# Kernel tuning notes

Hardware: AMD Instinct MI355X
Metric: run time of the kernel (lower is better)

## Reference

```python
import jax, jax.numpy as jnp
import numpy as np

N, E, D, L, G = 50000, 600000, 128, 3, 512
MAX_DIS = 5
BN_EPS = 1e-5


def _bn(z, g, b):
    # BatchNorm1d in training mode: biased batch statistics over axis 0
    mu = jnp.mean(z, axis=0)
    var = jnp.var(z, axis=0)
    return (z - mu) * jax.lax.rsqrt(var + BN_EPS) * g + b


def setup_inputs() -> dict:
    key = jax.random.key(0)
    ks = jax.random.split(key, 16)
    s = 0.05
    inp = {
        # int inputs
        'd': jax.random.randint(ks[0], (N,), 0, MAX_DIS + 1, dtype=jnp.int32),
        'src': jax.random.randint(ks[1], (E,), 0, N, dtype=jnp.int32),
        'dst': jax.random.randint(ks[2], (E,), 0, N, dtype=jnp.int32),
        'batch_ids': jnp.sort(jax.random.randint(ks[3], (N,), 0, G, dtype=jnp.int32)),
        # NodeEmbedding distance table
        'embed_d': jax.random.normal(ks[4], (MAX_DIS + 1, D)) * s,
        # per-layer params (stacked over L layers)
        'lin_W': jax.random.normal(ks[5], (L, D, D)) * s,   # self.linear weight (stored [in,out])
        'lin_b': jnp.zeros((L, D)),                          # self.linear bias
        'mlp_W1': jax.random.normal(ks[6], (L, D, D)) * s,   # MLP input linear (no bias, norm=True)
        'mlp_g1': jnp.ones((L, D)), 'mlp_b1': jnp.zeros((L, D)),  # MLP inner BN
        'mlp_W2': jax.random.normal(ks[7], (L, D, D)) * s,   # MLP output linear (no bias)
        'eps': jnp.zeros((L,)),                              # GIN eps per layer
        'bn_g': jnp.ones((L, D)), 'bn_b': jnp.zeros((L, D)), # LWL outer BN
        # Pool (gin=False, task='g')
        'pool_W1': jax.random.normal(ks[8], (D, D)) * s,
        'pool_g1': jnp.ones((D,)), 'pool_b1': jnp.zeros((D,)),
        'pool_W2': jax.random.normal(ks[9], (D, D)) * s,
        'pbn_g': jnp.ones((D,)), 'pbn_b': jnp.zeros((D,)),
        # predict MLP (norm=False -> biases, hdim=2*D, odim=num_tasks*num_classes=1)
        'pred_W1': jax.random.normal(ks[10], (D, 2 * D)) * s,
        'pred_b1': jnp.zeros((2 * D,)),
        'pred_W2': jax.random.normal(ks[11], (2 * D, 1)) * s,
        'pred_b2': jnp.zeros((1,)),
    }
    return inp


def reference(d, src, dst, batch_ids, embed_d, lin_W, lin_b,
              mlp_W1, mlp_g1, mlp_b1, mlp_W2, eps, bn_g, bn_b,
              pool_W1, pool_g1, pool_b1, pool_W2, pbn_g, pbn_b,
              pred_W1, pred_b1, pred_W2, pred_b2):
    # NodeEmbedding: x = embed_d(clamp(d, 0, max_dis))  (enc_a=None -> no feature encoder)
    x = embed_d[jnp.clip(d, 0, MAX_DIS)]                      # [N, D]

    counts = jax.ops.segment_sum(jnp.ones((N,), x.dtype), batch_ids, num_segments=G)
    denom = jnp.maximum(counts, 1.0)[:, None]                 # [G, 1]

    h_means = []
    for l in range(L):
        # L('vL'): message = relu(index_select(linear(x), src))  (enc_e=None)
        m = jax.nn.relu((x @ lin_W[l] + lin_b[l])[src])        # [E, D]
        # aggregate = scatter_add to dst over N nodes
        agg = jax.ops.segment_sum(m, dst, num_segments=N)      # [N, D]
        z = x * (1.0 + eps[l]) + agg                           # GIN eps residual
        # MLP(norm=True): Linear(no bias) -> BN -> ReLU -> Linear(no bias)
        h = jax.nn.relu(_bn(z @ mlp_W1[l], mlp_g1[l], mlp_b1[l])) @ mlp_W2[l]
        # LWL outer: x = relu(bn(xL))
        x = jax.nn.relu(_bn(h, bn_g[l], bn_b[l]))
        # global_mean_pool of this layer's output
        h_means.append(jax.ops.segment_sum(x, batch_ids, num_segments=G) / denom)

    # Pool (gin=False, task='g'); index_u is identity for plain MP, so scatter/gather are no-ops
    p = jax.nn.relu(_bn(x @ pool_W1, pool_g1, pool_b1)) @ pool_W2   # pooling MLP
    p = jax.nn.relu(_bn(p, pbn_g, pbn_b))
    h_graph = jax.ops.segment_sum(p, batch_ids, num_segments=G) / denom  # scatter mean
    # predict MLP (norm=False): Linear+bias -> ReLU -> Linear+bias
    prediction = jax.nn.relu(h_graph @ pred_W1 + pred_b1) @ pred_W2 + pred_b2  # [G, 1]

    return prediction, h_graph, jnp.stack(h_means)  # h_list stacked [L, G, D]
```

## Files before the change

kernel.cpp:

```cpp
#include <hip/hip_runtime.h>

typedef unsigned short ushort_t;
typedef __attribute__((ext_vector_type(8))) short bf16x8;
typedef __attribute__((ext_vector_type(4))) float f32x4;

#define NN 50000
#define NE 600000
#define DD 128
#define LL 3
#define GG 512
#define NB_SCAN 98
#define GGRID 782
#define SBK 16

__device__ __forceinline__ float b2f(ushort_t u){ return __uint_as_float(((unsigned)u)<<16); }
__device__ __forceinline__ ushort_t f2b(float f){
    unsigned x = __float_as_uint(f);
    return (ushort_t)((x + 0x7fffu + ((x>>16)&1u)) >> 16);
}

__global__ void k_mark(float* __restrict__ out, float val, int n){
    int i = blockIdx.x*256 + threadIdx.x; if (i >= n) return;
    out[i] = (i == 0) ? val : 0.f;
}

struct WPtrs { const float* p[11]; };
__global__ void k_setup(WPtrs wp, ushort_t* __restrict__ Wf,
                        const int* __restrict__ bids, int* __restrict__ goff,
                        int* __restrict__ cnt, float* __restrict__ banks,
                        const float* __restrict__ emb, const float* __restrict__ linW,
                        const float* __restrict__ linB, float* __restrict__ yrows){
    int idx = blockIdx.x*256 + threadIdx.x;
    if (idx < 180224){
        int m = idx >> 14, r = idx & 16383;
        int i = r & 7, l2 = (r >> 3) & 63, s = (r >> 9) & 3, n = r >> 11;
        int k   = s*32 + (l2 >> 4)*8 + i;
        int col = n*16 + (l2 & 15);
        Wf[idx] = f2b(wp.p[m][k*DD + col]);
    } else if (idx < 180737){
        int g = idx - 180224;
        int lo = 0, hi = NN;
        while (lo < hi){ int mid = (lo+hi) >> 1; if (bids[mid] < g) lo = mid+1; else hi = mid; }
        goff[g] = lo;
    } else if (idx < 230737){
        cnt[idx - 180737] = 0;
    } else if (idx < 263505){
        banks[idx - 230737] = 0.f;
    } else if (idx < 264273){
        int i = idx - 263505;
        int di = i >> 7, c = i & 127;
        float acc = linB[c];
        for (int k = 0; k < DD; k++) acc = fmaf(emb[di*DD + k], linW[k*DD + c], acc);
        yrows[i] = fmaxf(acc, 0.f);
    }
}

__global__ void k_count(const int* __restrict__ dst, int* __restrict__ cnt){
    int e4 = blockIdx.x*256 + threadIdx.x; if (e4 >= NE/4) return;
    int4 dv = ((const int4*)dst)[e4];
    atomicAdd(&cnt[dv.x], 1); atomicAdd(&cnt[dv.y], 1);
    atomicAdd(&cnt[dv.z], 1); atomicAdd(&cnt[dv.w], 1);
}
__global__ void k_scanA(const int* __restrict__ cnt, int* __restrict__ inc, int* __restrict__ bsum){
    __shared__ int s[512];
    int i = blockIdx.x*512 + threadIdx.x;
    int v = (i < NN) ? cnt[i] : 0;
    s[threadIdx.x] = v; __syncthreads();
    for (int off = 1; off < 512; off <<= 1){
        int add = (threadIdx.x >= off) ? s[threadIdx.x - off] : 0;
        __syncthreads();
        s[threadIdx.x] += add;
        __syncthreads();
    }
    if (i < NN) inc[i] = s[threadIdx.x];
    if (threadIdx.x == 511) bsum[blockIdx.x] = s[511];
}
__global__ void k_scanB(const int* __restrict__ bsum, int* __restrict__ boff){
    __shared__ int s[128];
    int t = threadIdx.x;
    int v = (t < NB_SCAN) ? bsum[t] : 0;
    s[t] = v; __syncthreads();
    for (int off = 1; off < 128; off <<= 1){
        int a = (t >= off) ? s[t - off] : 0;
        __syncthreads();
        s[t] += a;
        __syncthreads();
    }
    if (t < NB_SCAN) boff[t] = s[t] - v;
    if (t == NB_SCAN - 1) boff[NB_SCAN] = s[t];
}
__global__ void k_scanC(const int* __restrict__ cnt, const int* __restrict__ inc,
                        const int* __restrict__ boff, int* __restrict__ rowptr,
                        int* __restrict__ cursor){
    int i = blockIdx.x*512 + threadIdx.x;
    if (i < NN){
        int e = boff[blockIdx.x] + inc[i] - cnt[i];
        rowptr[i] = e; cursor[i] = e;
    } else if (i == NN){
        rowptr[NN] = NE;
    }
}
__global__ void k_fill(const int* __restrict__ src, const int* __restrict__ dst,
                       int* __restrict__ cursor, int* __restrict__ eidx){
    int e4 = blockIdx.x*256 + threadIdx.x; if (e4 >= NE/4) return;
    int4 dv = ((const int4*)dst)[e4];
    int4 sv = ((const int4*)src)[e4];
    int p0 = atomicAdd(&cursor[dv.x], 1); eidx[p0] = sv.x;
    int p1 = atomicAdd(&cursor[dv.y], 1); eidx[p1] = sv.y;
    int p2 = atomicAdd(&cursor[dv.z], 1); eidx[p2] = sv.z;
    int p3 = atomicAdd(&cursor[dv.w], 1); eidx[p3] = sv.w;
}

__global__ void k_agg0(const int* __restrict__ d, const float* __restrict__ emb,
                       const float* __restrict__ yrows,
                       const int* __restrict__ rowptr, const int* __restrict__ eidx,
                       const float* __restrict__ epsP, ushort_t* __restrict__ zb){
    __shared__ float eL[6*DD], yL[6*DD];
    int t = threadIdx.x;
    for (int i = t; i < 6*DD; i += 256){ eL[i] = emb[i]; yL[i] = yrows[i]; }
    __syncthreads();
    int node = blockIdx.x*16 + (t >> 4);
    if (node >= NN) return;
    int c8 = (t & 15) << 3;
    float epl = 1.0f + epsP[0];
    int dv = d[node]; dv = dv < 0 ? 0 : (dv > 5 ? 5 : dv);
    float a[8];
#pragma unroll
    for (int i = 0; i < 8; i++) a[i] = eL[dv*DD + c8 + i] * epl;
    int e0 = rowptr[node], e1 = rowptr[node+1];
    int e = e0;
    for (; e + 3 < e1; e += 4){
        int s0 = eidx[e], s1 = eidx[e+1], s2 = eidx[e+2], s3 = eidx[e+3];
        int c0 = d[s0], c1 = d[s1], c2 = d[s2], c3 = d[s3];
        c0 = c0 < 0 ? 0 : (c0 > 5 ? 5 : c0);
        c1 = c1 < 0 ? 0 : (c1 > 5 ? 5 : c1);
        c2 = c2 < 0 ? 0 : (c2 > 5 ? 5 : c2);
        c3 = c3 < 0 ? 0 : (c3 > 5 ? 5 : c3);
#pragma unroll
        for (int i = 0; i < 8; i++)
            a[i] += (yL[c0*DD + c8 + i] + yL[c1*DD + c8 + i])
                  + (yL[c2*DD + c8 + i] + yL[c3*DD + c8 + i]);
    }
    for (; e < e1; e++){
        int s = eidx[e];
        int c = d[s]; c = c < 0 ? 0 : (c > 5 ? 5 : c);
#pragma unroll
        for (int i = 0; i < 8; i++) a[i] += yL[c*DD + c8 + i];
    }
    bf16x8 o;
#pragma unroll
    for (int i = 0; i < 8; i++) o[i] = (short)f2b(a[i]);
    *(bf16x8*)(zb + (size_t)node*DD + c8) = o;
}

__global__ void k_agg(const ushort_t* __restrict__ xb, const ushort_t* __restrict__ yb,
                      ushort_t* __restrict__ zb,
                      const int* __restrict__ rowptr, const int* __restrict__ eidx,
                      const float* __restrict__ epsP, int l,
                      const float* __restrict__ banksIn, const float* __restrict__ bng,
                      const float* __restrict__ bnb){
    __shared__ float sst[256];
    int t = threadIdx.x;
    {
        float sv = 0.f;
#pragma unroll
        for (int b = 0; b < SBK; b++) sv += banksIn[(b << 8) + t];
        sst[t] = sv;
    }
    __syncthreads();
    int node = blockIdx.x*16 + (t >> 4);
    if (node >= NN) return;
    int c8 = (t & 15) << 3;
    float epl = 1.0f + epsP[l];
    bf16x8 xr = *(const bf16x8*)(xb + (size_t)node*DD + c8);
    float a[8];
#pragma unroll
    for (int i = 0; i < 8; i++){
        int c = c8 + i;
        float mu  = sst[c] * (1.0f/NN);
        float var = sst[c + DD] * (1.0f/NN) - mu*mu;
        float sc  = rsqrtf(fmaxf(var, 0.f) + 1e-5f) * bng[c];
        float sh  = bnb[c] - mu*sc;
        a[i] = fmaxf(fmaf(b2f((ushort_t)xr[i]), sc, sh), 0.f) * epl;
    }
    int e0 = rowptr[node], e1 = rowptr[node+1];
    int e = e0;
    for (; e + 3 < e1; e += 4){
        int s0 = eidx[e], s1 = eidx[e+1], s2 = eidx[e+2], s3 = eidx[e+3];
        bf16x8 v0 = *(const bf16x8*)(yb + (size_t)s0*DD + c8);
        bf16x8 v1 = *(const bf16x8*)(yb + (size_t)s1*DD + c8);
        bf16x8 v2 = *(const bf16x8*)(yb + (size_t)s2*DD + c8);
        bf16x8 v3 = *(const bf16x8*)(yb + (size_t)s3*DD + c8);
#pragma unroll
        for (int i = 0; i < 8; i++)
            a[i] += (b2f((ushort_t)v0[i]) + b2f((ushort_t)v1[i]))
                  + (b2f((ushort_t)v2[i]) + b2f((ushort_t)v3[i]));
    }
    for (; e < e1; e++){
        int s = eidx[e];
        bf16x8 v = *(const bf16x8*)(yb + (size_t)s*DD + c8);
#pragma unroll
        for (int i = 0; i < 8; i++) a[i] += b2f((ushort_t)v[i]);
    }
    bf16x8 o;
#pragma unroll
    for (int i = 0; i < 8; i++) o[i] = (short)f2b(a[i]);
    *(bf16x8*)(zb + (size_t)node*DD + c8) = o;
}

template<int AMODE, int OMODE, int STATS, int POOL>
__global__ __launch_bounds__(256) void k_gemm(
    const ushort_t* __restrict__ A, const ushort_t* __restrict__ Wf,
    const float* __restrict__ bias,
    const float* __restrict__ banksIn, const float* __restrict__ bng,
    const float* __restrict__ bnb,
    ushort_t* __restrict__ C, float* __restrict__ banksOut,
    const int* __restrict__ goff, float* __restrict__ pool_out, int M)
{
    __shared__ float ssl[256];
    __shared__ float sred[256];
    __shared__ float lrep[64*132];
    const int t = threadIdx.x;

    if (POOL && blockIdx.x >= GGRID){
        int g = blockIdx.x - GGRID;
        {
            float sv = 0.f;
#pragma unroll
            for (int b = 0; b < SBK; b++) sv += banksIn[(b << 8) + t];
            ssl[t] = sv;
        }
        __syncthreads();
        int c = t & 127, hf = t >> 7;
        float mu  = ssl[c] * (1.0f/NN);
        float var = ssl[c + DD] * (1.0f/NN) - mu*mu;
        float sc  = rsqrtf(fmaxf(var, 0.f) + 1e-5f) * bng[c];
        float sh  = bnb[c] - mu*sc;
        int r0 = goff[g], r1 = goff[g+1];
        float acc = 0.f;
        for (int r = r0 + hf; r < r1; r += 2)
            acc += fmaxf(fmaf(b2f(A[(size_t)r*DD + c]), sc, sh), 0.f);
        sred[t] = acc; __syncthreads();
        if (t < 128)
            pool_out[g*DD + t] = (sred[t] + sred[t+128]) / fmaxf((float)(r1 - r0), 1.0f);
        return;
    }

    const int w = t >> 6, l = t & 63;
    const int rowBlk = blockIdx.x*64, rowBase = rowBlk + w*16;
    const int lm = l & 15, kg = l >> 4;

    if (AMODE == 2){
        float sv = 0.f;
#pragma unroll
        for (int b = 0; b < SBK; b++) sv += banksIn[(b << 8) + t];
        ssl[t] = sv;
        __syncthreads();
        if (t < 128){
            float mu  = ssl[t] * (1.0f/NN);
            float var = ssl[t + DD] * (1.0f/NN) - mu*mu;
            float sc  = rsqrtf(fmaxf(var, 0.f) + 1e-5f) * bng[t];
            ssl[t] = sc;
            ssl[t + DD] = bnb[t] - mu*sc;
        }
    }
    if (STATS) sred[t] = 0.f;
    if (AMODE == 2 || STATS) __syncthreads();

    f32x4 acc[8];
#pragma unroll
    for (int n = 0; n < 8; n++) acc[n] = (f32x4){0.f,0.f,0.f,0.f};

    int arow = rowBase + lm;
    if (arow >= M) arow = M - 1;
    const ushort_t* aptr = A + (size_t)arow*DD + kg*8;

#pragma unroll
    for (int s = 0; s < 4; s++){
        bf16x8 af;
        if (AMODE == 0){
            af = *(const bf16x8*)(aptr + s*32);
        } else {
            bf16x8 ar = *(const bf16x8*)(aptr + s*32);
            int k0 = s*32 + kg*8;
#pragma unroll
            for (int i = 0; i < 8; i++){
                float v = b2f((ushort_t)ar[i]);
                v = fmaxf(fmaf(v, ssl[k0+i], ssl[DD+k0+i]), 0.f);
                ((ushort_t*)&af)[i] = f2b(v);
            }
        }
#pragma unroll
        for (int n = 0; n < 8; n++){
            bf16x8 bfr = *(const bf16x8*)(Wf + (size_t)((n*4 + s)*64 + l)*8);
            acc[n] = __builtin_amdgcn_mfma_f32_16x16x32_bf16(af, bfr, acc[n], 0, 0, 0);
        }
    }

#pragma unroll
    for (int n = 0; n < 8; n++){
        int col = n*16 + lm;
        float cs = 0.f, cq = 0.f;
#pragma unroll
        for (int j = 0; j < 4; j++){
            float v = acc[n][j];
            if (OMODE == 1) v = fmaxf(v + bias[col], 0.f);
            lrep[(w*16 + kg*4 + j)*132 + col] = v;
            if (STATS && (rowBase + kg*4 + j) < M){ cs += v; cq += v*v; }
        }
        if (STATS){
            cs += __shfl_xor(cs, 16); cs += __shfl_xor(cs, 32);
            cq += __shfl_xor(cq, 16); cq += __shfl_xor(cq, 32);
            if (kg == 0){
                atomicAdd(&sred[col], cs);
                atomicAdd(&sred[col + DD], cq);
            }
        }
    }
    __syncthreads();

    {
        int lr = t & 63;
        int gr = rowBlk + lr;
        if (gr < M){
            int seg = (t >> 6) * 32;
            const float* lp = lrep + lr*132 + seg;
            bf16x8 o0, o1, o2, o3;
#pragma unroll
            for (int i = 0; i < 8; i++){
                o0[i] = (short)f2b(lp[i]);
                o1[i] = (short)f2b(lp[8+i]);
                o2[i] = (short)f2b(lp[16+i]);
                o3[i] = (short)f2b(lp[24+i]);
            }
            ushort_t* cp = C + (size_t)gr*DD + seg;
            *(bf16x8*)(cp)      = o0;
            *(bf16x8*)(cp + 8)  = o1;
            *(bf16x8*)(cp + 16) = o2;
            *(bf16x8*)(cp + 24) = o3;
        }
    }

    if (STATS){
        __syncthreads();
        atomicAdd(&banksOut[((blockIdx.x & (SBK-1)) << 8) + t], sred[t]);
    }
}

__global__ __launch_bounds__(256) void k_poolpred(const ushort_t* __restrict__ zb,
        const float* __restrict__ banksIn, const float* __restrict__ bng,
        const float* __restrict__ bnb, const int* __restrict__ goff,
        const float* __restrict__ W1, const float* __restrict__ b1,
        const float* __restrict__ W2, const float* __restrict__ b2,
        float* __restrict__ out_hgraph, float* __restrict__ out_pred){
    __shared__ float hrow[DD];
    __shared__ float pr[256];
    int g = blockIdx.x, t = threadIdx.x;
    {
        float sv = 0.f;
#pragma unroll
        for (int b = 0; b < SBK; b++) sv += banksIn[(b << 8) + t];
        pr[t] = sv;
    }
    __syncthreads();
    int c = t & 127, hf = t >> 7;
    float mu  = pr[c] * (1.0f/NN);
    float var = pr[c + DD] * (1.0f/NN) - mu*mu;
    float sc  = rsqrtf(fmaxf(var, 0.f) + 1e-5f) * bng[c];
    float sh  = bnb[c] - mu*sc;
    __syncthreads();
    int r0 = goff[g], r1 = goff[g+1];
    float acc = 0.f;
    for (int r = r0 + hf; r < r1; r += 2)
        acc += fmaxf(fmaf(b2f(zb[(size_t)r*DD + c]), sc, sh), 0.f);
    pr[t] = acc; __syncthreads();
    if (t < 128){
        float m = (pr[t] + pr[t+128]) / fmaxf((float)(r1 - r0), 1.0f);
        hrow[t] = m;
        out_hgraph[g*DD + t] = m;
    }
    __syncthreads();
    float a2 = b1[t];
    for (int k = 0; k < DD; k++) a2 = fmaf(hrow[k], W1[k*256 + t], a2);
    pr[t] = fmaxf(a2, 0.f) * W2[t];
    __syncthreads();
    for (int off = 128; off > 0; off >>= 1){
        if (t < off) pr[t] += pr[t + off];
        __syncthreads();
    }
    if (t == 0) out_pred[g] = pr[0] + b2[0];
}

extern "C" void kernel_launch(void* const* d_in, const int* in_sizes, int n_in,
                              void* d_out, int out_size, void* d_ws, size_t ws_size,
                              hipStream_t stream){
    float* out = (float*)d_out;
    const int OUT_N = GG + GG*DD + LL*GG*DD;

    static const int EXP[24] = {50000,600000,600000,50000, 768,49152,384,49152,384,384,
                                49152,3,384,384,16384,128,128,16384,128,128,
                                32768,256,256,1};
    int bad = -1;
    if (n_in != 24) bad = 50;
    else for (int i = 0; i < 24; i++) if (in_sizes[i] != EXP[i]) { bad = i; break; }
    if (bad >= 0){
        k_mark<<<(OUT_N+255)/256, 256, 0, stream>>>(out, 2048.0f + (float)bad, OUT_N);
        return;
    }

    const int* d    = (const int*)d_in[0];
    const int* src  = (const int*)d_in[1];
    const int* dst  = (const int*)d_in[2];
    const int* bids = (const int*)d_in[3];
    const float* emb  = (const float*)d_in[4];
    const float* linW = (const float*)d_in[5];
    const float* linB = (const float*)d_in[6];
    const float* W1   = (const float*)d_in[7];
    const float* g1   = (const float*)d_in[8];
    const float* b1   = (const float*)d_in[9];
    const float* W2   = (const float*)d_in[10];
    const float* epsA = (const float*)d_in[11];
    const float* bng  = (const float*)d_in[12];
    const float* bnb  = (const float*)d_in[13];
    const float* pW1  = (const float*)d_in[14];
    const float* pg1  = (const float*)d_in[15];
    const float* pb1  = (const float*)d_in[16];
    const float* pW2  = (const float*)d_in[17];
    const float* pbng = (const float*)d_in[18];
    const float* pbnb = (const float*)d_in[19];
    const float* prW1 = (const float*)d_in[20];
    const float* prb1 = (const float*)d_in[21];
    const float* prW2 = (const float*)d_in[22];
    const float* prb2 = (const float*)d_in[23];

    ushort_t* xb  = (ushort_t*)d_ws;
    ushort_t* yb  = xb + (size_t)NN*DD;
    ushort_t* zb  = yb + (size_t)NN*DD;
    ushort_t* Wf  = zb + (size_t)NN*DD;
    float* SBANKS= (float*)(Wf + 11*16384);
    float* yrows = SBANKS + 8*SBK*256;
    int* cnt    = (int*)(yrows + 6*DD);
    int* inc    = cnt + NN;
    int* rowptr = inc + NN;
    int* cursor = rowptr + NN + 1;
    int* eidx   = cursor + NN;
    int* goff   = eidx + NE;
    int* bsum   = goff + GG + 1;
    int* boff   = bsum + NB_SCAN;

    float* out_pred   = out;
    float* out_hgraph = out + GG;
    float* out_hmeans = out + GG + GG*DD;

    const int AGG_GRID  = (NN + 15)/16;
    const int E4_GRID   = (NE/4 + 255)/256;
    const int SETUP_GRID= (264273 + 255)/256;
    const int GP_GRID   = GGRID + GG;

    WPtrs wp;
    for (int i = 0; i < 3; i++){
        wp.p[i]   = linW + (size_t)i*DD*DD;
        wp.p[3+i] = W1   + (size_t)i*DD*DD;
        wp.p[6+i] = W2   + (size_t)i*DD*DD;
    }
    wp.p[9] = pW1; wp.p[10] = pW2;
    const ushort_t* WfLin = Wf;
    const ushort_t* WfW1  = Wf + 3*16384;
    const ushort_t* WfW2  = Wf + 6*16384;
    const ushort_t* WfPW1 = Wf + 9*16384;
    const ushort_t* WfPW2 = Wf + 10*16384;

    float* BK0 = SBANKS + 0*SBK*256;
    float* BK1 = SBANKS + 1*SBK*256;
    float* BK5 = SBANKS + 5*SBK*256;
    float* BK6 = SBANKS + 6*SBK*256;
    float* BK7 = SBANKS + 7*SBK*256;

    k_setup<<<SETUP_GRID, 256, 0, stream>>>(wp, Wf, bids, goff, cnt, SBANKS,
                                            emb, linW, linB, yrows);
    k_count<<<E4_GRID, 256, 0, stream>>>(dst, cnt);
    k_scanA<<<NB_SCAN, 512, 0, stream>>>(cnt, inc, bsum);
    k_scanB<<<1, 128, 0, stream>>>(bsum, boff);
    k_scanC<<<NB_SCAN, 512, 0, stream>>>(cnt, inc, boff, rowptr, cursor);
    k_fill<<<E4_GRID, 256, 0, stream>>>(src, dst, cursor, eidx);

    k_agg0<<<AGG_GRID, 256, 0, stream>>>(d, emb, yrows, rowptr, eidx, epsA, zb);
    k_gemm<0,0,1,0><<<GGRID, 256, 0, stream>>>(zb, WfW1, nullptr, nullptr, nullptr, nullptr,
        yb, BK0, nullptr, nullptr, NN);
    k_gemm<2,0,1,0><<<GGRID, 256, 0, stream>>>(yb, WfW2, nullptr, BK0, g1, b1,
        xb, BK1, nullptr, nullptr, NN);

    for (int l = 1; l < LL; l++){
        float* pbank = SBANKS + (size_t)(2*l - 1)*SBK*256;
        float* bIn   = SBANKS + (size_t)(2*l)*SBK*256;
        float* bOut  = SBANKS + (size_t)(2*l + 1)*SBK*256;
        const float* pg = bng + (size_t)(l-1)*DD;
        const float* pb = bnb + (size_t)(l-1)*DD;

        k_gemm<2,1,0,1><<<GP_GRID, 256, 0, stream>>>(xb, WfLin + (size_t)l*16384,
            linB + (size_t)l*DD, pbank, pg, pb,
            yb, nullptr, goff, out_hmeans + (size_t)(l-1)*GG*DD, NN);
        k_agg<<<AGG_GRID, 256, 0, stream>>>(xb, yb, zb, rowptr, eidx, epsA, l, pbank, pg, pb);
        k_gemm<0,0,1,0><<<GGRID, 256, 0, stream>>>(zb, WfW1 + (size_t)l*16384, nullptr,
            nullptr, nullptr, nullptr, yb, bIn, nullptr, nullptr, NN);
        k_gemm<2,0,1,0><<<GGRID, 256, 0, stream>>>(yb, WfW2 + (size_t)l*16384, nullptr,
            bIn, g1 + (size_t)l*DD, b1 + (size_t)l*DD, xb, bOut, nullptr, nullptr, NN);
    }

    k_gemm<2,0,1,1><<<GP_GRID, 256, 0, stream>>>(xb, WfPW1, nullptr,
        BK5, bng + 2*DD, bnb + 2*DD,
        yb, BK6, goff, out_hmeans + (size_t)2*GG*DD, NN);
    k_gemm<2,0,1,0><<<GGRID, 256, 0, stream>>>(yb, WfPW2, nullptr,
        BK6, pg1, pb1, zb, BK7, nullptr, nullptr, NN);
    k_poolpred<<<GG, 256, 0, stream>>>(zb, BK7, pbng, pbnb, goff,
        prW1, prb1, prW2, prb2, out_hgraph, out_pred);
}
```

Baseline: 387.8 us.

## Halve GEMM row tile, split waves over columns, stage bf16 in LDS

The GEMM kernel now uses 32-row blocks, with the four waves arranged 2x2 over rows and column halves. Each wave holds 4 MFMA accumulators instead of 8. The output staging buffer in shared memory stores bf16 instead of fp32, so the write-back becomes plain vector copies and the block uses less LDS. The grid roughly doubles, and the statistics banks are increased to 32 to spread the atomic contention; setup zeroing and buffer offsets are adjusted to match. The aim is higher occupancy and less LDS traffic, at the cost of reloading the A tile per column half and possibly misaligned 16-byte LDS reads from the 132-element row stride.

```diff
diff --git a/kernel.cpp b/kernel.cpp
--- a/kernel.cpp
+++ b/kernel.cpp
@@ -10,8 +10,8 @@
 #define LL 3
 #define GG 512
 #define NB_SCAN 98
-#define GGRID 782
-#define SBK 16
+#define GGRID 1563
+#define SBK 32
 
 __device__ __forceinline__ float b2f(ushort_t u){ return __uint_as_float(((unsigned)u)<<16); }
 __device__ __forceinline__ ushort_t f2b(float f){
@@ -44,10 +44,10 @@
         goff[g] = lo;
     } else if (idx < 230737){
         cnt[idx - 180737] = 0;
-    } else if (idx < 263505){
+    } else if (idx < 296273){
         banks[idx - 230737] = 0.f;
-    } else if (idx < 264273){
-        int i = idx - 263505;
+    } else if (idx < 297041){
+        int i = idx - 296273;
         int di = i >> 7, c = i & 127;
         float acc = linB[c];
         for (int k = 0; k < DD; k++) acc = fmaf(emb[di*DD + k], linW[k*DD + c], acc);
@@ -219,7 +219,7 @@
 {
     __shared__ float ssl[256];
     __shared__ float sred[256];
-    __shared__ float lrep[64*132];
+    __shared__ ushort_t lrep[32*132];
     const int t = threadIdx.x;
 
     if (POOL && blockIdx.x >= GGRID){
@@ -247,7 +247,8 @@
     }
 
     const int w = t >> 6, l = t & 63;
-    const int rowBlk = blockIdx.x*64, rowBase = rowBlk + w*16;
+    const int rw = w >> 1, cw = w & 1;
+    const int rowBlk = blockIdx.x*32, rowBase = rowBlk + rw*16;
     const int lm = l & 15, kg = l >> 4;
 
     if (AMODE == 2){
@@ -267,9 +268,9 @@
     if (STATS) sred[t] = 0.f;
     if (AMODE == 2 || STATS) __syncthreads();
 
-    f32x4 acc[8];
-#pragma unroll
-    for (int n = 0; n < 8; n++) acc[n] = (f32x4){0.f,0.f,0.f,0.f};
+    f32x4 acc[4];
+#pragma unroll
+    for (int n = 0; n < 4; n++) acc[n] = (f32x4){0.f,0.f,0.f,0.f};
 
     int arow = rowBase + lm;
     if (arow >= M) arow = M - 1;
@@ -291,21 +292,22 @@
             }
         }
 #pragma unroll
-        for (int n = 0; n < 8; n++){
-            bf16x8 bfr = *(const bf16x8*)(Wf + (size_t)((n*4 + s)*64 + l)*8);
+        for (int n = 0; n < 4; n++){
+            int nc = cw*4 + n;
+            bf16x8 bfr = *(const bf16x8*)(Wf + (size_t)((nc*4 + s)*64 + l)*8);
             acc[n] = __builtin_amdgcn_mfma_f32_16x16x32_bf16(af, bfr, acc[n], 0, 0, 0);
         }
     }
 
 #pragma unroll
-    for (int n = 0; n < 8; n++){
-        int col = n*16 + lm;
+    for (int n = 0; n < 4; n++){
+        int col = (cw*4 + n)*16 + lm;
         float cs = 0.f, cq = 0.f;
 #pragma unroll
         for (int j = 0; j < 4; j++){
             float v = acc[n][j];
             if (OMODE == 1) v = fmaxf(v + bias[col], 0.f);
-            lrep[(w*16 + kg*4 + j)*132 + col] = v;
+            lrep[(rw*16 + kg*4 + j)*132 + col] = f2b(v);
             if (STATS && (rowBase + kg*4 + j) < M){ cs += v; cq += v*v; }
         }
         if (STATS){
@@ -320,24 +322,16 @@
     __syncthreads();
 
     {
-        int lr = t & 63;
+        int lr = t >> 3;
         int gr = rowBlk + lr;
         if (gr < M){
-            int seg = (t >> 6) * 32;
-            const float* lp = lrep + lr*132 + seg;
-            bf16x8 o0, o1, o2, o3;
-#pragma unroll
-            for (int i = 0; i < 8; i++){
-                o0[i] = (short)f2b(lp[i]);
-                o1[i] = (short)f2b(lp[8+i]);
-                o2[i] = (short)f2b(lp[16+i]);
-                o3[i] = (short)f2b(lp[24+i]);
-            }
+            int seg = (t & 7) * 16;
+            const ushort_t* lp = lrep + lr*132 + seg;
+            bf16x8 o0 = *(const bf16x8*)(lp);
+            bf16x8 o1 = *(const bf16x8*)(lp + 8);
             ushort_t* cp = C + (size_t)gr*DD + seg;
-            *(bf16x8*)(cp)      = o0;
-            *(bf16x8*)(cp + 8)  = o1;
-            *(bf16x8*)(cp + 16) = o2;
-            *(bf16x8*)(cp + 24) = o3;
+            *(bf16x8*)(cp)     = o0;
+            *(bf16x8*)(cp + 8) = o1;
         }
     }
 
@@ -454,7 +448,7 @@
 
     const int AGG_GRID  = (NN + 15)/16;
     const int E4_GRID   = (NE/4 + 255)/256;
-    const int SETUP_GRID= (264273 + 255)/256;
+    const int SETUP_GRID= (297041 + 255)/256;
     const int GP_GRID   = GGRID + GG;
 
     WPtrs wp;
```

After: 372.3 us. -4.0%, faster.
